# Performance work log

Measured on AMD Instinct MI355X. Metric: run time of the kernel, lower is better.

Reference implementation:

```python
import jax, jax.numpy as jnp
import numpy as np

S = 64.0   # arcface scale
M = 0.5    # arcface additive angular margin
EPS = 1e-07
B, D, C = 1024, 512, 100000


def setup_inputs() -> dict:
    key = jax.random.key(0)
    k1, k2, k3 = jax.random.split(key, 3)
    features = jax.random.normal(k1, (B, D), dtype=jnp.float32)
    # Linear(512, 100000, bias=False) weight, ~1/sqrt(512) init scale.
    W = jax.random.normal(k2, (C, D), dtype=jnp.float32) * 0.04
    y_true = jax.random.randint(k3, (B,), 0, C, dtype=jnp.int64)
    return {"features": features, "W": W, "y_true": y_true}


def reference(features, W, y_true):
    # L2-normalize features along dim=1 (torch F.normalize, eps=1e-12).
    norm = jnp.maximum(jnp.linalg.norm(features, axis=1, keepdims=True), 1e-12)
    xn = features / norm
    # NOTE: the original module's weight-normalization loop is a no-op
    # (rebinds a local), so W is used unnormalized — faithful to the source.
    wf = xn @ W.T                                   # [B, C] cosine-like logits
    tgt = wf[jnp.arange(B), y_true]                  # true-class logit per row
    # arcface: s * cos(acos(clamp(t)) + m)
    numerator = S * jnp.cos(jnp.arccos(jnp.clip(tgt, -1.0 + EPS, 1.0 - EPS)) + M)
    # exp-sum over all classes except the true one (mask instead of python-loop concat)
    not_true = jnp.arange(C)[None, :] != y_true[:, None]   # [B, C]
    excl_sum = jnp.sum(jnp.where(not_true, jnp.exp(S * wf), 0.0), axis=1)
    denominator = jnp.exp(numerator) + excl_sum
    L = numerator - jnp.log(denominator)
    return -jnp.mean(L)
```

## Files before the change

kernel.cpp:

```cpp
#include <hip/hip_runtime.h>
#include <math.h>

#define BATCH 1024
#define DIM   512
#define NCLS  100000
#define SCALE_S 64.0f
#define MARGIN  0.5f
#define EPS_REF 1e-7f
#define SEXP 92.332482616893656878f

#define NSLAB 64
#define NBLK  1563
#define CHUNK 16
#define NCHUNK_WAVE 16
#define NRSCOPY 8

typedef __attribute__((ext_vector_type(4))) float floatx4;
typedef __attribute__((ext_vector_type(2))) long  longx2;

#if __has_builtin(__builtin_amdgcn_exp2f)
#define EXP2(x) __builtin_amdgcn_exp2f(x)
#else
#define EXP2(x) exp2f(x)
#endif

__device__ __forceinline__ float red16(float v) {
    v += __shfl_xor(v, 1);
    v += __shfl_xor(v, 2);
    v += __shfl_xor(v, 4);
    v += __shfl_xor(v, 8);
    return v;
}

__global__ __launch_bounds__(256)
void k_prep(const float* __restrict__ features,
            const float* __restrict__ W,
            const int* __restrict__ y,
            unsigned char* __restrict__ xf8,
            float* __restrict__ rowsum,
            float* __restrict__ tgt) {
    const int row = blockIdx.x;
    const int t = threadIdx.x;
    const int lane = t & 63;
    const int wave = t >> 6;
    __shared__ float redS[4], redD[4];

    const float2 v  = *(const float2*)(features + (size_t)row * DIM + t * 2);
    const float2 wv = *(const float2*)(W + (size_t)y[row] * DIM + t * 2);
    float ss = v.x * v.x + v.y * v.y;
    float dd = v.x * wv.x + v.y * wv.y;
    #pragma unroll
    for (int m = 32; m >= 1; m >>= 1) { ss += __shfl_xor(ss, m); dd += __shfl_xor(dd, m); }
    if (lane == 0) { redS[wave] = ss; redD[wave] = dd; }
    __syncthreads();
    const float tot  = redS[0] + redS[1] + redS[2] + redS[3];
    const float dtot = redD[0] + redD[1] + redD[2] + redD[3];
    const float nrm = fmaxf(sqrtf(tot), 1e-12f);
    const float sc = SEXP / nrm;

    int pk = __builtin_amdgcn_cvt_pk_fp8_f32(v.x * sc, v.y * sc, 0, false);
    const int k0 = t * 2;
    const int off = ((k0 & 31) >> 3) * 128 + (k0 >> 5) * 8 + (k0 & 7);
    *(unsigned short*)(xf8 + (size_t)row * DIM + off) = (unsigned short)(pk & 0xFFFF);

    if (t < NRSCOPY) rowsum[t * BATCH + row] = 0.0f;
    if (t == 0) tgt[row] = dtot / nrm;
}


#define LBK(ni,kk) { const int r_ = (ni)*16 + l15;                             \
    const int cs_ = (kk)*2 + qh;                                               \
    Bf[ni][kk] = *(const long*)(&Ws[r_*DIM + (((cs_)^(r_&7))<<4) + ql8]); }

#define LB16(ni) LBK(ni,0) LBK(ni,1) LBK(ni,2)  LBK(ni,3)  LBK(ni,4)  LBK(ni,5)  LBK(ni,6)  LBK(ni,7) \
                 LBK(ni,8) LBK(ni,9) LBK(ni,10) LBK(ni,11) LBK(ni,12) LBK(ni,13) LBK(ni,14) LBK(ni,15)

#define LA(Ab, c) { const unsigned char* p_ = abase + (size_t)(c) * (CHUNK * DIM); \
    Ab[0] = *(const longx2*)(p_ +  0); Ab[1] = *(const longx2*)(p_ + 16);      \
    Ab[2] = *(const longx2*)(p_ + 32); Ab[3] = *(const longx2*)(p_ + 48);      \
    Ab[4] = *(const longx2*)(p_ + 64); Ab[5] = *(const longx2*)(p_ + 80);      \
    Ab[6] = *(const longx2*)(p_ + 96); Ab[7] = *(const longx2*)(p_ + 112); }

#define STEP(Ab, kk) { const long av_ = Ab[(kk)>>1][(kk)&1];                   \
    acc0 = __builtin_amdgcn_mfma_f32_16x16x32_fp8_fp8(av_, Bf[0][kk], acc0, 0, 0, 0); \
    acc1 = __builtin_amdgcn_mfma_f32_16x16x32_fp8_fp8(av_, Bf[1][kk], acc1, 0, 0, 0); \
    acc2 = __builtin_amdgcn_mfma_f32_16x16x32_fp8_fp8(av_, Bf[2][kk], acc2, 0, 0, 0); \
    acc3 = __builtin_amdgcn_mfma_f32_16x16x32_fp8_fp8(av_, Bf[3][kk], acc3, 0, 0, 0); }

#define EPI(reg) { float p_;                                                   \
    if (full) { p_ = EXP2(acc0[reg]) + EXP2(acc1[reg])                         \
                   + EXP2(acc2[reg]) + EXP2(acc3[reg]); }                      \
    else { p_ = 0.f;                                                           \
        if (n0 +      l15 < NCLS) p_ += EXP2(acc0[reg]);                       \
        if (n0 + 16 + l15 < NCLS) p_ += EXP2(acc1[reg]);                       \
        if (n0 + 32 + l15 < NCLS) p_ += EXP2(acc2[reg]);                       \
        if (n0 + 48 + l15 < NCLS) p_ += EXP2(acc3[reg]); }                     \
    p_ = red16(p_);                                                            \
    if (l15 == 0) atomicAdd(&rs[rowb_ + (reg)], p_); }

#define COMPUTE(Ab, c) {                                                       \
    floatx4 acc0 = (floatx4){0.f,0.f,0.f,0.f};                                 \
    floatx4 acc1 = (floatx4){0.f,0.f,0.f,0.f};                                 \
    floatx4 acc2 = (floatx4){0.f,0.f,0.f,0.f};                                 \
    floatx4 acc3 = (floatx4){0.f,0.f,0.f,0.f};                                 \
    STEP(Ab,0)  STEP(Ab,1)  STEP(Ab,2)  STEP(Ab,3)                             \
    STEP(Ab,4)  STEP(Ab,5)  STEP(Ab,6)  STEP(Ab,7)                             \
    STEP(Ab,8)  STEP(Ab,9)  STEP(Ab,10) STEP(Ab,11)                            \
    STEP(Ab,12) STEP(Ab,13) STEP(Ab,14) STEP(Ab,15)                            \
    const int rowb_ = (wave * NCHUNK_WAVE + (c)) * CHUNK + quad * 4;           \
    EPI(0) EPI(1) EPI(2) EPI(3) }

__global__ __launch_bounds__(256, 2)
void k_gemm_fused(const float* __restrict__ W,
                  const unsigned char* __restrict__ xf8,
                  float* __restrict__ rowsum) {
    __shared__ __align__(16) unsigned char Ws[NSLAB * DIM];

    const int tid  = threadIdx.x;
    const int wave = tid >> 6;
    const int lane = tid & 63;
    const int quad = lane >> 4;
    const int l15  = lane & 15;
    const int qh   = quad >> 1;
    const int ql8  = (quad & 1) << 3;
    const int n0   = blockIdx.x * NSLAB;
    float* rs = rowsum + (blockIdx.x & (NRSCOPY - 1)) * BATCH;

    const unsigned char* abase =
        xf8 + (size_t)(wave * NCHUNK_WAVE * CHUNK + l15) * DIM + quad * 128;

    longx2 A0[8], A1[8];
    LA(A0, 0)

    #pragma unroll
    for (int j = 0; j < 8; ++j) {
        const int c  = j * 256 + tid;
        const int r  = c >> 5;
        const int cs = c & 31;
        int rg = n0 + r; if (rg > NCLS - 1) rg = NCLS - 1;
        const float4* s4 = (const float4*)(W + (size_t)rg * DIM + cs * 16);
        const float4 f0 = s4[0], f1 = s4[1], f2 = s4[2], f3 = s4[3];
        int w0 = __builtin_amdgcn_cvt_pk_fp8_f32(f0.x, f0.y, 0, false);
        w0     = __builtin_amdgcn_cvt_pk_fp8_f32(f0.z, f0.w, w0, true);
        int w1 = __builtin_amdgcn_cvt_pk_fp8_f32(f1.x, f1.y, 0, false);
        w1     = __builtin_amdgcn_cvt_pk_fp8_f32(f1.z, f1.w, w1, true);
        int w2 = __builtin_amdgcn_cvt_pk_fp8_f32(f2.x, f2.y, 0, false);
        w2     = __builtin_amdgcn_cvt_pk_fp8_f32(f2.z, f2.w, w2, true);
        int w3 = __builtin_amdgcn_cvt_pk_fp8_f32(f3.x, f3.y, 0, false);
        w3     = __builtin_amdgcn_cvt_pk_fp8_f32(f3.z, f3.w, w3, true);
        *(int4*)(&Ws[r * DIM + ((cs ^ (r & 7)) << 4)]) = make_int4(w0, w1, w2, w3);
    }
    __syncthreads();

    long Bf[4][16];
    LB16(0) LB16(1) LB16(2) LB16(3)

    const bool full = (n0 + NSLAB <= NCLS);

    #pragma unroll 1
    for (int c = 0; c < NCHUNK_WAVE; c += 2) {
        LA(A1, c + 1)
        COMPUTE(A0, c)
        const int cn = (c + 2 < NCHUNK_WAVE) ? c + 2 : 0;
        LA(A0, cn)
        COMPUTE(A1, c + 1)
    }
}

__global__ void k_finalize(const float* __restrict__ rowsum,
                           const float* __restrict__ tgt,
                           float* __restrict__ out) {
    const int tid = threadIdx.x;
    const int lane = tid & 63;
    const int wave = tid >> 6;
    __shared__ float red[4];

    float s = 0.f;
    #pragma unroll
    for (int i = 0; i < 4; ++i) {
        const int b = tid + i * 256;
        float rsum = 0.f;
        #pragma unroll
        for (int cp = 0; cp < NRSCOPY; ++cp) rsum += rowsum[cp * BATCH + b];
        const float traw = tgt[b];
        const float tc = fminf(fmaxf(traw, -1.0f + EPS_REF), 1.0f - EPS_REF);
        const float num = SCALE_S * cosf(acosf(tc) + MARGIN);
        const float excl = rsum - expf(SCALE_S * traw);
        const float denom = expf(num) + excl;
        s += num - logf(denom);
    }
    #pragma unroll
    for (int m = 32; m >= 1; m >>= 1) s += __shfl_xor(s, m);
    if (lane == 0) red[wave] = s;
    __syncthreads();
    if (tid == 0)
        out[0] = -(red[0] + red[1] + red[2] + red[3]) / (float)BATCH;
}

extern "C" void kernel_launch(void* const* d_in, const int* in_sizes, int n_in,
                              void* d_out, int out_size, void* d_ws, size_t ws_size,
                              hipStream_t stream) {
    const float* features = (const float*)d_in[0];
    const float* W        = (const float*)d_in[1];
    const int*   y        = (const int*)d_in[2];
    float* out = (float*)d_out;

    const size_t XF8_BYTES = (size_t)BATCH * DIM;
    const size_t RS_BYTES  = (size_t)NRSCOPY * BATCH * sizeof(float);
    char* ws = (char*)d_ws;
    unsigned char* xf8 = (unsigned char*)ws;
    float* rowsum = (float*)(ws + XF8_BYTES);
    float* tgt    = (float*)(ws + XF8_BYTES + RS_BYTES);

    k_prep<<<BATCH, 256, 0, stream>>>(features, W, y, xf8, rowsum, tgt);
    k_gemm_fused<<<NBLK, 256, 0, stream>>>(W, xf8, rowsum);
    k_finalize<<<1, 256, 0, stream>>>(rowsum, tgt, out);
}
```

Baseline: 396.4 us.

## Stream B fragments from LDS per step instead of holding them in registers

The W slab was kept as 64 long registers per thread. It is now re-read from shared memory inside every MFMA step with 16-byte loads, using a re-permuted LDS layout so each load feeds two K-steps. Freeing those registers allows launch bounds of 3 blocks per SM for more occupancy. In exchange, every chunk now issues repeated LDS reads, which adds LDS bandwidth pressure and latency inside the MFMA loop.

After: 468.0 us. +18.1%, slower.

```diff
diff --git a/kernel.cpp b/kernel.cpp
--- a/kernel.cpp
+++ b/kernel.cpp
@@ -68,24 +68,27 @@
 }
 
 
-#define LBK(ni,kk) { const int r_ = (ni)*16 + l15;                             \
-    const int cs_ = (kk)*2 + qh;                                               \
-    Bf[ni][kk] = *(const long*)(&Ws[r_*DIM + (((cs_)^(r_&7))<<4) + ql8]); }
-
-#define LB16(ni) LBK(ni,0) LBK(ni,1) LBK(ni,2)  LBK(ni,3)  LBK(ni,4)  LBK(ni,5)  LBK(ni,6)  LBK(ni,7) \
-                 LBK(ni,8) LBK(ni,9) LBK(ni,10) LBK(ni,11) LBK(ni,12) LBK(ni,13) LBK(ni,14) LBK(ni,15)
+#define STEPJ(Ab, jj) {                                                        \
+    const longx2 q0 = *(const longx2*)(&Ws[0 * 8192 + bbase + (((jj) ^ swb) << 4)]); \
+    const longx2 q1 = *(const longx2*)(&Ws[1 * 8192 + bbase + (((jj) ^ swb) << 4)]); \
+    const longx2 q2 = *(const longx2*)(&Ws[2 * 8192 + bbase + (((jj) ^ swb) << 4)]); \
+    const longx2 q3 = *(const longx2*)(&Ws[3 * 8192 + bbase + (((jj) ^ swb) << 4)]); \
+    const long a0 = Ab[jj][0];                                                 \
+    const long a1 = Ab[jj][1];                                                 \
+    acc0 = __builtin_amdgcn_mfma_f32_16x16x32_fp8_fp8(a0, q0[0], acc0, 0, 0, 0); \
+    acc1 = __builtin_amdgcn_mfma_f32_16x16x32_fp8_fp8(a0, q1[0], acc1, 0, 0, 0); \
+    acc2 = __builtin_amdgcn_mfma_f32_16x16x32_fp8_fp8(a0, q2[0], acc2, 0, 0, 0); \
+    acc3 = __builtin_amdgcn_mfma_f32_16x16x32_fp8_fp8(a0, q3[0], acc3, 0, 0, 0); \
+    acc0 = __builtin_amdgcn_mfma_f32_16x16x32_fp8_fp8(a1, q0[1], acc0, 0, 0, 0); \
+    acc1 = __builtin_amdgcn_mfma_f32_16x16x32_fp8_fp8(a1, q1[1], acc1, 0, 0, 0); \
+    acc2 = __builtin_amdgcn_mfma_f32_16x16x32_fp8_fp8(a1, q2[1], acc2, 0, 0, 0); \
+    acc3 = __builtin_amdgcn_mfma_f32_16x16x32_fp8_fp8(a1, q3[1], acc3, 0, 0, 0); }
 
 #define LA(Ab, c) { const unsigned char* p_ = abase + (size_t)(c) * (CHUNK * DIM); \
     Ab[0] = *(const longx2*)(p_ +  0); Ab[1] = *(const longx2*)(p_ + 16);      \
     Ab[2] = *(const longx2*)(p_ + 32); Ab[3] = *(const longx2*)(p_ + 48);      \
     Ab[4] = *(const longx2*)(p_ + 64); Ab[5] = *(const longx2*)(p_ + 80);      \
     Ab[6] = *(const longx2*)(p_ + 96); Ab[7] = *(const longx2*)(p_ + 112); }
-
-#define STEP(Ab, kk) { const long av_ = Ab[(kk)>>1][(kk)&1];                   \
-    acc0 = __builtin_amdgcn_mfma_f32_16x16x32_fp8_fp8(av_, Bf[0][kk], acc0, 0, 0, 0); \
-    acc1 = __builtin_amdgcn_mfma_f32_16x16x32_fp8_fp8(av_, Bf[1][kk], acc1, 0, 0, 0); \
-    acc2 = __builtin_amdgcn_mfma_f32_16x16x32_fp8_fp8(av_, Bf[2][kk], acc2, 0, 0, 0); \
-    acc3 = __builtin_amdgcn_mfma_f32_16x16x32_fp8_fp8(av_, Bf[3][kk], acc3, 0, 0, 0); }
 
 #define EPI(reg) { float p_;                                                   \
     if (full) { p_ = EXP2(acc0[reg]) + EXP2(acc1[reg])                         \
@@ -103,14 +106,12 @@
     floatx4 acc1 = (floatx4){0.f,0.f,0.f,0.f};                                 \
     floatx4 acc2 = (floatx4){0.f,0.f,0.f,0.f};                                 \
     floatx4 acc3 = (floatx4){0.f,0.f,0.f,0.f};                                 \
-    STEP(Ab,0)  STEP(Ab,1)  STEP(Ab,2)  STEP(Ab,3)                             \
-    STEP(Ab,4)  STEP(Ab,5)  STEP(Ab,6)  STEP(Ab,7)                             \
-    STEP(Ab,8)  STEP(Ab,9)  STEP(Ab,10) STEP(Ab,11)                            \
-    STEP(Ab,12) STEP(Ab,13) STEP(Ab,14) STEP(Ab,15)                            \
+    STEPJ(Ab,0) STEPJ(Ab,1) STEPJ(Ab,2) STEPJ(Ab,3)                            \
+    STEPJ(Ab,4) STEPJ(Ab,5) STEPJ(Ab,6) STEPJ(Ab,7)                            \
     const int rowb_ = (wave * NCHUNK_WAVE + (c)) * CHUNK + quad * 4;           \
     EPI(0) EPI(1) EPI(2) EPI(3) }
 
-__global__ __launch_bounds__(256, 2)
+__global__ __launch_bounds__(256, 3)
 void k_gemm_fused(const float* __restrict__ W,
                   const unsigned char* __restrict__ xf8,
                   float* __restrict__ rowsum) {
@@ -121,11 +122,12 @@
     const int lane = tid & 63;
     const int quad = lane >> 4;
     const int l15  = lane & 15;
-    const int qh   = quad >> 1;
-    const int ql8  = (quad & 1) << 3;
     const int n0   = blockIdx.x * NSLAB;
     float* rs = rowsum + (blockIdx.x & (NRSCOPY - 1)) * BATCH;
 
+    const int bbase = l15 * 512 + quad * 128;
+    const int swb   = l15 & 7;
+
     const unsigned char* abase =
         xf8 + (size_t)(wave * NCHUNK_WAVE * CHUNK + l15) * DIM + quad * 128;
 
@@ -134,26 +136,29 @@
 
     #pragma unroll
     for (int j = 0; j < 8; ++j) {
-        const int c  = j * 256 + tid;
-        const int r  = c >> 5;
-        const int cs = c & 31;
+        const int c   = j * 256 + tid;
+        const int r   = c >> 5;
+        const int rem = c & 31;
+        const int jj  = rem >> 2;
+        const int qd  = rem & 3;
         int rg = n0 + r; if (rg > NCLS - 1) rg = NCLS - 1;
-        const float4* s4 = (const float4*)(W + (size_t)rg * DIM + cs * 16);
-        const float4 f0 = s4[0], f1 = s4[1], f2 = s4[2], f3 = s4[3];
-        int w0 = __builtin_amdgcn_cvt_pk_fp8_f32(f0.x, f0.y, 0, false);
-        w0     = __builtin_amdgcn_cvt_pk_fp8_f32(f0.z, f0.w, w0, true);
-        int w1 = __builtin_amdgcn_cvt_pk_fp8_f32(f1.x, f1.y, 0, false);
-        w1     = __builtin_amdgcn_cvt_pk_fp8_f32(f1.z, f1.w, w1, true);
-        int w2 = __builtin_amdgcn_cvt_pk_fp8_f32(f2.x, f2.y, 0, false);
-        w2     = __builtin_amdgcn_cvt_pk_fp8_f32(f2.z, f2.w, w2, true);
-        int w3 = __builtin_amdgcn_cvt_pk_fp8_f32(f3.x, f3.y, 0, false);
-        w3     = __builtin_amdgcn_cvt_pk_fp8_f32(f3.z, f3.w, w3, true);
-        *(int4*)(&Ws[r * DIM + ((cs ^ (r & 7)) << 4)]) = make_int4(w0, w1, w2, w3);
+        const float* src = W + (size_t)rg * DIM + jj * 64 + qd * 8;
+        const float4 e0 = *(const float4*)(src);
+        const float4 e1 = *(const float4*)(src + 4);
+        const float4 o0 = *(const float4*)(src + 32);
+        const float4 o1 = *(const float4*)(src + 36);
+        int w0 = __builtin_amdgcn_cvt_pk_fp8_f32(e0.x, e0.y, 0, false);
+        w0     = __builtin_amdgcn_cvt_pk_fp8_f32(e0.z, e0.w, w0, true);
+        int w1 = __builtin_amdgcn_cvt_pk_fp8_f32(e1.x, e1.y, 0, false);
+        w1     = __builtin_amdgcn_cvt_pk_fp8_f32(e1.z, e1.w, w1, true);
+        int w2 = __builtin_amdgcn_cvt_pk_fp8_f32(o0.x, o0.y, 0, false);
+        w2     = __builtin_amdgcn_cvt_pk_fp8_f32(o0.z, o0.w, w2, true);
+        int w3 = __builtin_amdgcn_cvt_pk_fp8_f32(o1.x, o1.y, 0, false);
+        w3     = __builtin_amdgcn_cvt_pk_fp8_f32(o1.z, o1.w, w3, true);
+        *(int4*)(&Ws[r * 512 + ((qd * 8 + (jj ^ (r & 7))) << 4)]) =
+            make_int4(w0, w1, w2, w3);
     }
     __syncthreads();
-
-    long Bf[4][16];
-    LB16(0) LB16(1) LB16(2) LB16(3)
 
     const bool full = (n0 + NSLAB <= NCLS);
 
```
